# Performance work log

Hardware: AMD Instinct MI355X
Metric: run time of the kernel (lower is better)

The kernel has to match this reference:

```python
import jax, jax.numpy as jnp
import numpy as np

NEG_INF = -1.0e9  # matches torch masked_fill_ value


def setup_inputs() -> dict:
    key = jax.random.key(0)
    kq, kk, kv, km = jax.random.split(key, 4)
    B, H, S, D = 4, 16, 2048, 64
    Q = jax.random.normal(kq, (B, H, S, D), dtype=jnp.float32)
    K = jax.random.normal(kk, (B, H, S, D), dtype=jnp.float32)
    V = jax.random.normal(kv, (B, H, S, D), dtype=jnp.float32)
    attn_mask = jax.random.randint(km, (B, 1, 1, S), 0, 2).astype(jnp.bool_)
    return {"Q": Q, "K": K, "V": V, "attn_mask": attn_mask}


def reference(Q, K, V, attn_mask):
    d_k = Q.shape[-1]
    scale = 1.0 / jnp.sqrt(jnp.asarray(d_k, dtype=Q.dtype))
    # scores: [B, H, Sq, Sk]
    scores = jnp.einsum('bhqd,bhkd->bhqk', Q, K) * scale
    scores = jnp.where(attn_mask, jnp.asarray(NEG_INF, dtype=scores.dtype), scores)
    attn = jax.nn.softmax(scores, axis=-1)
    context = jnp.einsum('bhqk,bhkd->bhqd', attn, V)
    return (context, attn)
```

## Files before the change

### kernel.cpp

```cpp
#include <hip/hip_runtime.h>
#include <stdint.h>

#define B_    4
#define H_    16
#define S_    2048
#define D_    64
#define SCALE_LOG2E 0.1803368801111244f

typedef __bf16 bf16x8 __attribute__((ext_vector_type(8)));
typedef __bf16 bf16x4 __attribute__((ext_vector_type(4)));
typedef float  f32x4  __attribute__((ext_vector_type(4)));

__global__ __launch_bounds__(256)
void prep_k(const float* __restrict__ K, __bf16* __restrict__ img) {
    int t = blockIdx.x * 256 + threadIdx.x;
    int C = t & 255, slice = t >> 8;
    int sb = slice & 1, e = (slice >> 1) & 31, bh = slice >> 6;
    int l15 = C & 15, lhi = (C >> 4) & 3, kd = (C >> 6) & 1, ksub = C >> 7;
    const float* src = K + (((size_t)bh * S_ + e * 64 + sb * 32 + ksub * 16 + l15) * D_
                            + kd * 32 + lhi * 8);
    float4 a = *reinterpret_cast<const float4*>(src);
    float4 b = *reinterpret_cast<const float4*>(src + 4);
    bf16x8 w = { (__bf16)a.x,(__bf16)a.y,(__bf16)a.z,(__bf16)a.w,
                 (__bf16)b.x,(__bf16)b.y,(__bf16)b.z,(__bf16)b.w };
    *reinterpret_cast<bf16x8*>((char*)img + ((size_t)t << 4)) = w;
}

__global__ __launch_bounds__(256)
void prep_v(const float* __restrict__ V, __bf16* __restrict__ img) {
    __shared__ float Ls[64][65];
    const int tid = threadIdx.x;
    const int bh = blockIdx.x >> 5, e = blockIdx.x & 31;
    const float* Vp = V + ((size_t)bh * S_ + e * 64) * D_;
    for (int i = tid; i < 1024; i += 256) {
        int r = i >> 4, c = (i & 15) << 2;
        float4 v = reinterpret_cast<const float4*>(Vp)[i];
        Ls[r][c] = v.x; Ls[r][c+1] = v.y; Ls[r][c+2] = v.z; Ls[r][c+3] = v.w;
    }
    __syncthreads();
    char* base = (char*)img + (size_t)(bh * 32 + e) * 8192;
    #pragma unroll
    for (int m = tid; m < 512; m += 256) {
        int sb = m >> 8, C2 = m & 255;
        int db = C2 >> 6, lhi = (C2 >> 4) & 3, l15 = C2 & 15;
        bf16x8 w;
        #pragma unroll
        for (int j = 0; j < 8; ++j)
            w[j] = (__bf16)Ls[sb * 32 + lhi * 4 + (j & 3) + ((j >> 2) << 4)][db * 16 + l15];
        *reinterpret_cast<bf16x8*>(base + sb * 4096 + C2 * 16) = w;
    }
}

__global__ __launch_bounds__(256, 2)
void sdpa_main(const float* __restrict__ Q, const __bf16* __restrict__ Kimg,
               const __bf16* __restrict__ Vimg, const int* __restrict__ mask,
               float* __restrict__ ctx_out, float* __restrict__ attn_out)
{
    __shared__ __align__(16) float shbuf[64 * 65];

    const int tid  = threadIdx.x;
    const int lane = tid & 63, wid = tid >> 6;
    const int l15  = lane & 15, lhi = lane >> 4;
    const int par  = wid & 1;
    const int sb   = wid >> 1;

    const int orig = blockIdx.x, cpx = gridDim.x >> 3;
    const int bid  = (orig & 7) * cpx + (orig >> 3);
    const int qt = bid & 31, bh = bid >> 5, b = bh >> 4;

    const char* kimgT = (const char*)Kimg + (size_t)bh * 262144;
    const char* vimgT = (const char*)Vimg + (size_t)bh * 262144;

    bf16x8 bQ[4][2];
    #pragma unroll
    for (int rb = 0; rb < 4; ++rb) {
        const float* qrow = Q + ((size_t)bh * S_ + qt * 64 + rb * 16 + l15) * D_ + lhi * 8;
        float4 a = *reinterpret_cast<const float4*>(qrow);
        float4 c = *reinterpret_cast<const float4*>(qrow + 4);
        bf16x8 w0 = { (__bf16)(a.x*SCALE_LOG2E),(__bf16)(a.y*SCALE_LOG2E),
                      (__bf16)(a.z*SCALE_LOG2E),(__bf16)(a.w*SCALE_LOG2E),
                      (__bf16)(c.x*SCALE_LOG2E),(__bf16)(c.y*SCALE_LOG2E),
                      (__bf16)(c.z*SCALE_LOG2E),(__bf16)(c.w*SCALE_LOG2E) };
        bQ[rb][0] = w0;
        a = *reinterpret_cast<const float4*>(qrow + 32);
        c = *reinterpret_cast<const float4*>(qrow + 36);
        bf16x8 w1 = { (__bf16)(a.x*SCALE_LOG2E),(__bf16)(a.y*SCALE_LOG2E),
                      (__bf16)(a.z*SCALE_LOG2E),(__bf16)(a.w*SCALE_LOG2E),
                      (__bf16)(c.x*SCALE_LOG2E),(__bf16)(c.y*SCALE_LOG2E),
                      (__bf16)(c.z*SCALE_LOG2E),(__bf16)(c.w*SCALE_LOG2E) };
        bQ[rb][1] = w1;
    }

    uint32_t mwv[4] = {0, 0, 0, 0};
    {
        const int* mrow = mask + b * S_ + sb * 32 + lhi * 4;
        #pragma unroll
        for (int tt = 0; tt < 16; ++tt) {
            int e = (((tt + qt) & 15) << 1) | par;
            #pragma unroll
            for (int ksub = 0; ksub < 2; ++ksub) {
                int4 mm = *reinterpret_cast<const int4*>(mrow + e * 64 + ksub * 16);
                uint32_t nib = (mm.x ? 1u : 0u) | (mm.y ? 2u : 0u) |
                               (mm.z ? 4u : 0u) | (mm.w ? 8u : 0u);
                mwv[tt >> 2] |= nib << (((tt & 3) * 8) + ksub * 4);
            }
        }
    }

    bf16x8 kf[2][2][2];
    auto loadK = [&](int bufi, int tt) {
        int e = (((tt + qt) & 15) << 1) | par;
        const char* p = kimgT + (size_t)(e * 2 + sb) * 4096 + lane * 16;
        kf[bufi][0][0] = *reinterpret_cast<const bf16x8*>(p);
        kf[bufi][0][1] = *reinterpret_cast<const bf16x8*>(p + 1024);
        kf[bufi][1][0] = *reinterpret_cast<const bf16x8*>(p + 2048);
        kf[bufi][1][1] = *reinterpret_cast<const bf16x8*>(p + 3072);
    };
    bf16x8 vv[2][4];
    auto loadV = [&](int bufi, int tt) {
        int e = (((tt + qt) & 15) << 1) | par;
        const char* p = vimgT + (size_t)(e * 2 + sb) * 4096 + lane * 16;
        vv[bufi][0] = *reinterpret_cast<const bf16x8*>(p);
        vv[bufi][1] = *reinterpret_cast<const bf16x8*>(p + 1024);
        vv[bufi][2] = *reinterpret_cast<const bf16x8*>(p + 2048);
        vv[bufi][3] = *reinterpret_cast<const bf16x8*>(p + 3072);
    };

    float ls[4] = {0.f, 0.f, 0.f, 0.f};
    loadK(0, 0);
    #pragma unroll
    for (int tt = 0; tt < 16; ++tt) {
        if (tt + 1 < 16) loadK((tt + 1) & 1, tt + 1);
        const int cur = tt & 1;
        #pragma unroll
        for (int ksub = 0; ksub < 2; ++ksub) {
            uint32_t nib = (mwv[tt >> 2] >> (((tt & 3) * 8) + ksub * 4)) & 15u;
            #pragma unroll
            for (int rb = 0; rb < 4; ++rb) {
                f32x4 acc = {0.f, 0.f, 0.f, 0.f};
                acc = __builtin_amdgcn_mfma_f32_16x16x32_bf16(kf[cur][ksub][0], bQ[rb][0], acc, 0, 0, 0);
                acc = __builtin_amdgcn_mfma_f32_16x16x32_bf16(kf[cur][ksub][1], bQ[rb][1], acc, 0, 0, 0);
                float p0 = (nib & 1u) ? 0.f : exp2f(acc[0]);
                float p1 = (nib & 2u) ? 0.f : exp2f(acc[1]);
                float p2 = (nib & 4u) ? 0.f : exp2f(acc[2]);
                float p3 = (nib & 8u) ? 0.f : exp2f(acc[3]);
                ls[rb] += (p0 + p1) + (p2 + p3);
            }
        }
    }

    #pragma unroll
    for (int rb = 0; rb < 4; ++rb) {
        ls[rb] += __shfl_xor(ls[rb], 16);
        ls[rb] += __shfl_xor(ls[rb], 32);
    }
    if (lhi == 0) {
        #pragma unroll
        for (int rb = 0; rb < 4; ++rb) shbuf[(wid * 4 + rb) * 16 + l15] = ls[rb];
    }
    __syncthreads();
    float rl[4];
    #pragma unroll
    for (int rb = 0; rb < 4; ++rb) {
        float tot = (shbuf[rb * 16 + l15] + shbuf[(4 + rb) * 16 + l15]) +
                    (shbuf[(8 + rb) * 16 + l15] + shbuf[(12 + rb) * 16 + l15]);
        rl[rb] = 1.0f / tot;
    }

    f32x4 ctx[4][4];
    #pragma unroll
    for (int rb = 0; rb < 4; ++rb)
        #pragma unroll
        for (int db = 0; db < 4; ++db) ctx[rb][db] = (f32x4){0.f, 0.f, 0.f, 0.f};

    const size_t arowq = (size_t)bh * S_ + (size_t)qt * 64;

    loadK(0, 0); loadV(0, 0);
    bf16x4 pk[2][4];
    #pragma unroll
    for (int tt = 0; tt < 16; ++tt) {
        if (tt + 1 < 16) { loadK((tt + 1) & 1, tt + 1); loadV((tt + 1) & 1, tt + 1); }
        const int cur = tt & 1;
        const int e = (((tt + qt) & 15) << 1) | par;
        const int colbase = e * 64 + sb * 32;
        #pragma unroll
        for (int rb = 0; rb < 4; ++rb) {
            float* arow = attn_out + (arowq + rb * 16 + l15) * S_ + colbase + lhi * 4;
            #pragma unroll
            for (int ksub = 0; ksub < 2; ++ksub) {
                uint32_t nib = (mwv[tt >> 2] >> (((tt & 3) * 8) + ksub * 4)) & 15u;
                f32x4 acc = {0.f, 0.f, 0.f, 0.f};
                acc = __builtin_amdgcn_mfma_f32_16x16x32_bf16(kf[cur][ksub][0], bQ[rb][0], acc, 0, 0, 0);
                acc = __builtin_amdgcn_mfma_f32_16x16x32_bf16(kf[cur][ksub][1], bQ[rb][1], acc, 0, 0, 0);
                float p0 = (nib & 1u) ? 0.f : exp2f(acc[0]) * rl[rb];
                float p1 = (nib & 2u) ? 0.f : exp2f(acc[1]) * rl[rb];
                float p2 = (nib & 4u) ? 0.f : exp2f(acc[2]) * rl[rb];
                float p3 = (nib & 8u) ? 0.f : exp2f(acc[3]) * rl[rb];
                float4 st = { p0, p1, p2, p3 };
                *reinterpret_cast<float4*>(arow + ksub * 16) = st;
                bf16x4 pkk = { (__bf16)p0, (__bf16)p1, (__bf16)p2, (__bf16)p3 };
                pk[ksub][rb] = pkk;
            }
        }
        #pragma unroll
        for (int db = 0; db < 4; ++db) {
            #pragma unroll
            for (int rb = 0; rb < 4; ++rb) {
                bf16x8 Av;
                Av[0]=pk[0][rb][0]; Av[1]=pk[0][rb][1]; Av[2]=pk[0][rb][2]; Av[3]=pk[0][rb][3];
                Av[4]=pk[1][rb][0]; Av[5]=pk[1][rb][1]; Av[6]=pk[1][rb][2]; Av[7]=pk[1][rb][3];
                ctx[rb][db] = __builtin_amdgcn_mfma_f32_16x16x32_bf16(Av, vv[cur][db], ctx[rb][db], 0, 0, 0);
            }
        }
    }

    __syncthreads();
    for (int ph = 0; ph < 4; ++ph) {
        if (wid == ph) {
            #pragma unroll
            for (int rb = 0; rb < 4; ++rb)
                #pragma unroll
                for (int db = 0; db < 4; ++db)
                    #pragma unroll
                    for (int r = 0; r < 4; ++r) {
                        float* c = &shbuf[(rb * 16 + lhi * 4 + r) * 65 + db * 16 + l15];
                        if (ph == 0) *c = ctx[rb][db][r];
                        else         *c += ctx[rb][db][r];
                    }
        }
        __syncthreads();
    }
    for (int i = tid; i < 4096; i += 256) {
        int q = i >> 6, d = i & 63;
        ctx_out[(arowq + q) * D_ + d] = shbuf[q * 65 + d];
    }
}

extern "C" void kernel_launch(void* const* d_in, const int* in_sizes, int n_in,
                              void* d_out, int out_size, void* d_ws, size_t ws_size,
                              hipStream_t stream) {
    const float* Q    = (const float*)d_in[0];
    const float* K    = (const float*)d_in[1];
    const float* V    = (const float*)d_in[2];
    const int*   mask = (const int*)d_in[3];

    float* ctx_out  = (float*)d_out;
    float* attn_out = ctx_out + (size_t)B_ * H_ * S_ * D_;

    __bf16* Kimg = (__bf16*)d_ws;
    __bf16* Vimg = Kimg + (size_t)B_ * H_ * S_ * D_;

    prep_k<<<4096, 256, 0, stream>>>(K, Kimg);
    prep_v<<<B_ * H_ * 32, 256, 0, stream>>>(V, Vimg);
    sdpa_main<<<B_ * H_ * 32, 256, 0, stream>>>(Q, Kimg, Vimg, mask, ctx_out, attn_out);
}
```

Baseline: 438.2 us.

## Restructure attention into single-wave blocks over 16 query rows each

Replaces the 256-thread block, in which four waves split the keys of 64 queries and reduce through shared memory, with 64-thread blocks where one wave handles 16 query rows across all keys. This removes the shared-memory row-sum and context reductions and their barriers, and launches four times as many blocks. The attention-probability stores become nontemporal. The trade-off is that each wave now re-reads the full K and V for only 16 queries, so cache traffic per query goes up.

```diff
diff --git a/kernel.cpp b/kernel.cpp
--- a/kernel.cpp
+++ b/kernel.cpp
@@ -51,188 +51,192 @@
     }
 }
 
-__global__ __launch_bounds__(256, 2)
+__global__ __launch_bounds__(64, 3)
 void sdpa_main(const float* __restrict__ Q, const __bf16* __restrict__ Kimg,
                const __bf16* __restrict__ Vimg, const int* __restrict__ mask,
                float* __restrict__ ctx_out, float* __restrict__ attn_out)
 {
-    __shared__ __align__(16) float shbuf[64 * 65];
-
-    const int tid  = threadIdx.x;
-    const int lane = tid & 63, wid = tid >> 6;
-    const int l15  = lane & 15, lhi = lane >> 4;
-    const int par  = wid & 1;
-    const int sb   = wid >> 1;
-
-    const int orig = blockIdx.x, cpx = gridDim.x >> 3;
-    const int bid  = (orig & 7) * cpx + (orig >> 3);
-    const int qt = bid & 31, bh = bid >> 5, b = bh >> 4;
+    const int lane = threadIdx.x;
+    const int l15 = lane & 15, lhi = lane >> 4;
+
+    const int orig = blockIdx.x;
+    const int bid = (orig & 7) * (int)(gridDim.x >> 3) + (orig >> 3);
+    const int q16 = bid & 127, bh = bid >> 7, b = bh >> 4;
 
     const char* kimgT = (const char*)Kimg + (size_t)bh * 262144;
     const char* vimgT = (const char*)Vimg + (size_t)bh * 262144;
 
-    bf16x8 bQ[4][2];
-    #pragma unroll
-    for (int rb = 0; rb < 4; ++rb) {
-        const float* qrow = Q + ((size_t)bh * S_ + qt * 64 + rb * 16 + l15) * D_ + lhi * 8;
+    bf16x8 bQ0, bQ1;
+    {
+        const float* qrow = Q + ((size_t)bh * S_ + q16 * 16 + l15) * D_ + lhi * 8;
         float4 a = *reinterpret_cast<const float4*>(qrow);
         float4 c = *reinterpret_cast<const float4*>(qrow + 4);
-        bf16x8 w0 = { (__bf16)(a.x*SCALE_LOG2E),(__bf16)(a.y*SCALE_LOG2E),
-                      (__bf16)(a.z*SCALE_LOG2E),(__bf16)(a.w*SCALE_LOG2E),
-                      (__bf16)(c.x*SCALE_LOG2E),(__bf16)(c.y*SCALE_LOG2E),
-                      (__bf16)(c.z*SCALE_LOG2E),(__bf16)(c.w*SCALE_LOG2E) };
-        bQ[rb][0] = w0;
+        bQ0 = (bf16x8){ (__bf16)(a.x*SCALE_LOG2E),(__bf16)(a.y*SCALE_LOG2E),
+                        (__bf16)(a.z*SCALE_LOG2E),(__bf16)(a.w*SCALE_LOG2E),
+                        (__bf16)(c.x*SCALE_LOG2E),(__bf16)(c.y*SCALE_LOG2E),
+                        (__bf16)(c.z*SCALE_LOG2E),(__bf16)(c.w*SCALE_LOG2E) };
         a = *reinterpret_cast<const float4*>(qrow + 32);
         c = *reinterpret_cast<const float4*>(qrow + 36);
-        bf16x8 w1 = { (__bf16)(a.x*SCALE_LOG2E),(__bf16)(a.y*SCALE_LOG2E),
-                      (__bf16)(a.z*SCALE_LOG2E),(__bf16)(a.w*SCALE_LOG2E),
-                      (__bf16)(c.x*SCALE_LOG2E),(__bf16)(c.y*SCALE_LOG2E),
-                      (__bf16)(c.z*SCALE_LOG2E),(__bf16)(c.w*SCALE_LOG2E) };
-        bQ[rb][1] = w1;
-    }
-
-    uint32_t mwv[4] = {0, 0, 0, 0};
+        bQ1 = (bf16x8){ (__bf16)(a.x*SCALE_LOG2E),(__bf16)(a.y*SCALE_LOG2E),
+                        (__bf16)(a.z*SCALE_LOG2E),(__bf16)(a.w*SCALE_LOG2E),
+                        (__bf16)(c.x*SCALE_LOG2E),(__bf16)(c.y*SCALE_LOG2E),
+                        (__bf16)(c.z*SCALE_LOG2E),(__bf16)(c.w*SCALE_LOG2E) };
+    }
+
+    uint32_t mA0,mA1,mA2,mA3, mB0,mB1,mB2,mB3, mC0,mC1,mC2,mC3, mD0,mD1,mD2,mD3;
     {
-        const int* mrow = mask + b * S_ + sb * 32 + lhi * 4;
+        const int* mb2 = mask + b * S_ + lhi * 4;
+        auto packw = [&](int tw, uint32_t& a, uint32_t& bb, uint32_t& cc, uint32_t& dd) {
+            a = bb = cc = dd = 0;
+            #pragma unroll
+            for (int u = 0; u < 8; ++u) {
+                int e = (tw * 8 + u + q16) & 31;
+                const int* p = mb2 + e * 64;
+                int4 m0 = *reinterpret_cast<const int4*>(p);
+                int4 m1 = *reinterpret_cast<const int4*>(p + 16);
+                int4 m2 = *reinterpret_cast<const int4*>(p + 32);
+                int4 m3 = *reinterpret_cast<const int4*>(p + 48);
+                uint32_t nA = (m0.x?1u:0u)|(m0.y?2u:0u)|(m0.z?4u:0u)|(m0.w?8u:0u);
+                uint32_t nB = (m1.x?1u:0u)|(m1.y?2u:0u)|(m1.z?4u:0u)|(m1.w?8u:0u);
+                uint32_t nC = (m2.x?1u:0u)|(m2.y?2u:0u)|(m2.z?4u:0u)|(m2.w?8u:0u);
+                uint32_t nD = (m3.x?1u:0u)|(m3.y?2u:0u)|(m3.z?4u:0u)|(m3.w?8u:0u);
+                a |= nA << (u*4); bb |= nB << (u*4); cc |= nC << (u*4); dd |= nD << (u*4);
+            }
+        };
+        packw(0, mA0, mB0, mC0, mD0);
+        packw(1, mA1, mB1, mC1, mD1);
+        packw(2, mA2, mB2, mC2, mD2);
+        packw(3, mA3, mB3, mC3, mD3);
+    }
+
+    bf16x8 kf[2][2][2];
+    auto loadK = [&](int tt) {
+        int e = (tt + q16) & 31;
+        const char* p0 = kimgT + (size_t)(e * 2) * 4096 + lane * 16;
+        kf[0][0][0] = *reinterpret_cast<const bf16x8*>(p0);
+        kf[0][0][1] = *reinterpret_cast<const bf16x8*>(p0 + 1024);
+        kf[0][1][0] = *reinterpret_cast<const bf16x8*>(p0 + 2048);
+        kf[0][1][1] = *reinterpret_cast<const bf16x8*>(p0 + 3072);
+        const char* p1 = p0 + 4096;
+        kf[1][0][0] = *reinterpret_cast<const bf16x8*>(p1);
+        kf[1][0][1] = *reinterpret_cast<const bf16x8*>(p1 + 1024);
+        kf[1][1][0] = *reinterpret_cast<const bf16x8*>(p1 + 2048);
+        kf[1][1][1] = *reinterpret_cast<const bf16x8*>(p1 + 3072);
+    };
+    bf16x8 vv[2][4];
+    auto loadV = [&](int tt) {
+        int e = (tt + q16) & 31;
+        const char* p0 = vimgT + (size_t)(e * 2) * 4096 + lane * 16;
+        vv[0][0] = *reinterpret_cast<const bf16x8*>(p0);
+        vv[0][1] = *reinterpret_cast<const bf16x8*>(p0 + 1024);
+        vv[0][2] = *reinterpret_cast<const bf16x8*>(p0 + 2048);
+        vv[0][3] = *reinterpret_cast<const bf16x8*>(p0 + 3072);
+        const char* p1 = p0 + 4096;
+        vv[1][0] = *reinterpret_cast<const bf16x8*>(p1);
+        vv[1][1] = *reinterpret_cast<const bf16x8*>(p1 + 1024);
+        vv[1][2] = *reinterpret_cast<const bf16x8*>(p1 + 2048);
+        vv[1][3] = *reinterpret_cast<const bf16x8*>(p1 + 3072);
+    };
+
+    float ls = 0.f;
+    loadK(0);
+    auto sumExp = [&](const f32x4& acc, uint32_t nib) -> float {
+        float p0 = (nib & 1u) ? 0.f : exp2f(acc[0]);
+        float p1 = (nib & 2u) ? 0.f : exp2f(acc[1]);
+        float p2 = (nib & 4u) ? 0.f : exp2f(acc[2]);
+        float p3 = (nib & 8u) ? 0.f : exp2f(acc[3]);
+        return (p0 + p1) + (p2 + p3);
+    };
+    auto pass1_8 = [&](int tw, uint32_t mA, uint32_t mB, uint32_t mC, uint32_t mD) {
+        #pragma unroll 2
+        for (int u = 0; u < 8; ++u) {
+            int tt = tw * 8 + u;
+            f32x4 z = {0.f,0.f,0.f,0.f};
+            f32x4 a00 = __builtin_amdgcn_mfma_f32_16x16x32_bf16(kf[0][0][0], bQ0, z, 0,0,0);
+            a00 = __builtin_amdgcn_mfma_f32_16x16x32_bf16(kf[0][0][1], bQ1, a00, 0,0,0);
+            f32x4 a01 = __builtin_amdgcn_mfma_f32_16x16x32_bf16(kf[0][1][0], bQ0, z, 0,0,0);
+            a01 = __builtin_amdgcn_mfma_f32_16x16x32_bf16(kf[0][1][1], bQ1, a01, 0,0,0);
+            f32x4 a10 = __builtin_amdgcn_mfma_f32_16x16x32_bf16(kf[1][0][0], bQ0, z, 0,0,0);
+            a10 = __builtin_amdgcn_mfma_f32_16x16x32_bf16(kf[1][0][1], bQ1, a10, 0,0,0);
+            f32x4 a11 = __builtin_amdgcn_mfma_f32_16x16x32_bf16(kf[1][1][0], bQ0, z, 0,0,0);
+            a11 = __builtin_amdgcn_mfma_f32_16x16x32_bf16(kf[1][1][1], bQ1, a11, 0,0,0);
+            loadK((tt + 1) & 31);
+            int sh = u * 4;
+            ls += sumExp(a00, (mA >> sh) & 15u) + sumExp(a01, (mB >> sh) & 15u)
+                + sumExp(a10, (mC >> sh) & 15u) + sumExp(a11, (mD >> sh) & 15u);
+        }
+    };
+    pass1_8(0, mA0, mB0, mC0, mD0);
+    pass1_8(1, mA1, mB1, mC1, mD1);
+    pass1_8(2, mA2, mB2, mC2, mD2);
+    pass1_8(3, mA3, mB3, mC3, mD3);
+
+    ls += __shfl_xor(ls, 16);
+    ls += __shfl_xor(ls, 32);
+    const float rl = 1.0f / ls;
+
+    f32x4 ctx[4];
+    #pragma unroll
+    for (int db = 0; db < 4; ++db) ctx[db] = (f32x4){0.f,0.f,0.f,0.f};
+
+    const size_t arow0 = (size_t)bh * S_ + (size_t)q16 * 16;
+    float* arowp = attn_out + (arow0 + l15) * S_ + lhi * 4;
+
+    loadK(0); loadV(0);
+    auto pass2_8 = [&](int tw, uint32_t mA, uint32_t mB, uint32_t mC, uint32_t mD) {
+        #pragma unroll 2
+        for (int u = 0; u < 8; ++u) {
+            int tt = tw * 8 + u;
+            int e = (tt + q16) & 31;
+            f32x4 z = {0.f,0.f,0.f,0.f};
+            f32x4 a00 = __builtin_amdgcn_mfma_f32_16x16x32_bf16(kf[0][0][0], bQ0, z, 0,0,0);
+            a00 = __builtin_amdgcn_mfma_f32_16x16x32_bf16(kf[0][0][1], bQ1, a00, 0,0,0);
+            f32x4 a01 = __builtin_amdgcn_mfma_f32_16x16x32_bf16(kf[0][1][0], bQ0, z, 0,0,0);
+            a01 = __builtin_amdgcn_mfma_f32_16x16x32_bf16(kf[0][1][1], bQ1, a01, 0,0,0);
+            f32x4 a10 = __builtin_amdgcn_mfma_f32_16x16x32_bf16(kf[1][0][0], bQ0, z, 0,0,0);
+            a10 = __builtin_amdgcn_mfma_f32_16x16x32_bf16(kf[1][0][1], bQ1, a10, 0,0,0);
+            f32x4 a11 = __builtin_amdgcn_mfma_f32_16x16x32_bf16(kf[1][1][0], bQ0, z, 0,0,0);
+            a11 = __builtin_amdgcn_mfma_f32_16x16x32_bf16(kf[1][1][1], bQ1, a11, 0,0,0);
+            loadK((tt + 1) & 31);
+            int sh = u * 4;
+            uint32_t nA = (mA >> sh) & 15u, nB = (mB >> sh) & 15u;
+            uint32_t nC = (mC >> sh) & 15u, nD = (mD >> sh) & 15u;
+            f32x4 sA = { (nA&1u)?0.f:exp2f(a00[0])*rl, (nA&2u)?0.f:exp2f(a00[1])*rl,
+                         (nA&4u)?0.f:exp2f(a00[2])*rl, (nA&8u)?0.f:exp2f(a00[3])*rl };
+            f32x4 sB = { (nB&1u)?0.f:exp2f(a01[0])*rl, (nB&2u)?0.f:exp2f(a01[1])*rl,
+                         (nB&4u)?0.f:exp2f(a01[2])*rl, (nB&8u)?0.f:exp2f(a01[3])*rl };
+            f32x4 sC = { (nC&1u)?0.f:exp2f(a10[0])*rl, (nC&2u)?0.f:exp2f(a10[1])*rl,
+                         (nC&4u)?0.f:exp2f(a10[2])*rl, (nC&8u)?0.f:exp2f(a10[3])*rl };
+            f32x4 sD = { (nD&1u)?0.f:exp2f(a11[0])*rl, (nD&2u)?0.f:exp2f(a11[1])*rl,
+                         (nD&4u)?0.f:exp2f(a11[2])*rl, (nD&8u)?0.f:exp2f(a11[3])*rl };
+            float* ap = arowp + e * 64;
+            __builtin_nontemporal_store(sA, reinterpret_cast<f32x4*>(ap));
+            __builtin_nontemporal_store(sB, reinterpret_cast<f32x4*>(ap + 16));
+            __builtin_nontemporal_store(sC, reinterpret_cast<f32x4*>(ap + 32));
+            __builtin_nontemporal_store(sD, reinterpret_cast<f32x4*>(ap + 48));
+            bf16x8 Av0 = { (__bf16)sA[0],(__bf16)sA[1],(__bf16)sA[2],(__bf16)sA[3],
+                           (__bf16)sB[0],(__bf16)sB[1],(__bf16)sB[2],(__bf16)sB[3] };
+            bf16x8 Av1 = { (__bf16)sC[0],(__bf16)sC[1],(__bf16)sC[2],(__bf16)sC[3],
+                           (__bf16)sD[0],(__bf16)sD[1],(__bf16)sD[2],(__bf16)sD[3] };
+            #pragma unroll
+            for (int db = 0; db < 4; ++db) {
+                ctx[db] = __builtin_amdgcn_mfma_f32_16x16x32_bf16(Av0, vv[0][db], ctx[db], 0,0,0);
+                ctx[db] = __builtin_amdgcn_mfma_f32_16x16x32_bf16(Av1, vv[1][db], ctx[db], 0,0,0);
+            }
+            loadV((tt + 1) & 31);
+        }
+    };
+    pass2_8(0, mA0, mB0, mC0, mD0);
+    pass2_8(1, mA1, mB1, mC1, mD1);
+    pass2_8(2, mA2, mB2, mC2, mD2);
+    pass2_8(3, mA3, mB3, mC3, mD3);
+
+    #pragma unroll
+    for (int db = 0; db < 4; ++db) {
         #pragma unroll
-        for (int tt = 0; tt < 16; ++tt) {
-            int e = (((tt + qt) & 15) << 1) | par;
-            #pragma unroll
-            for (int ksub = 0; ksub < 2; ++ksub) {
-                int4 mm = *reinterpret_cast<const int4*>(mrow + e * 64 + ksub * 16);
-                uint32_t nib = (mm.x ? 1u : 0u) | (mm.y ? 2u : 0u) |
-                               (mm.z ? 4u : 0u) | (mm.w ? 8u : 0u);
-                mwv[tt >> 2] |= nib << (((tt & 3) * 8) + ksub * 4);
-            }
+        for (int r = 0; r < 4; ++r) {
+            ctx_out[(arow0 + lhi * 4 + r) * D_ + db * 16 + l15] = ctx[db][r];
         }
-    }
-
-    bf16x8 kf[2][2][2];
-    auto loadK = [&](int bufi, int tt) {
-        int e = (((tt + qt) & 15) << 1) | par;
-        const char* p = kimgT + (size_t)(e * 2 + sb) * 4096 + lane * 16;
-        kf[bufi][0][0] = *reinterpret_cast<const bf16x8*>(p);
-        kf[bufi][0][1] = *reinterpret_cast<const bf16x8*>(p + 1024);
-        kf[bufi][1][0] = *reinterpret_cast<const bf16x8*>(p + 2048);
-        kf[bufi][1][1] = *reinterpret_cast<const bf16x8*>(p + 3072);
-    };
-    bf16x8 vv[2][4];
-    auto loadV = [&](int bufi, int tt) {
-        int e = (((tt + qt) & 15) << 1) | par;
-        const char* p = vimgT + (size_t)(e * 2 + sb) * 4096 + lane * 16;
-        vv[bufi][0] = *reinterpret_cast<const bf16x8*>(p);
-        vv[bufi][1] = *reinterpret_cast<const bf16x8*>(p + 1024);
-        vv[bufi][2] = *reinterpret_cast<const bf16x8*>(p + 2048);
-        vv[bufi][3] = *reinterpret_cast<const bf16x8*>(p + 3072);
-    };
-
-    float ls[4] = {0.f, 0.f, 0.f, 0.f};
-    loadK(0, 0);
-    #pragma unroll
-    for (int tt = 0; tt < 16; ++tt) {
-        if (tt + 1 < 16) loadK((tt + 1) & 1, tt + 1);
-        const int cur = tt & 1;
-        #pragma unroll
-        for (int ksub = 0; ksub < 2; ++ksub) {
-            uint32_t nib = (mwv[tt >> 2] >> (((tt & 3) * 8) + ksub * 4)) & 15u;
-            #pragma unroll
-            for (int rb = 0; rb < 4; ++rb) {
-                f32x4 acc = {0.f, 0.f, 0.f, 0.f};
-                acc = __builtin_amdgcn_mfma_f32_16x16x32_bf16(kf[cur][ksub][0], bQ[rb][0], acc, 0, 0, 0);
-                acc = __builtin_amdgcn_mfma_f32_16x16x32_bf16(kf[cur][ksub][1], bQ[rb][1], acc, 0, 0, 0);
-                float p0 = (nib & 1u) ? 0.f : exp2f(acc[0]);
-                float p1 = (nib & 2u) ? 0.f : exp2f(acc[1]);
-                float p2 = (nib & 4u) ? 0.f : exp2f(acc[2]);
-                float p3 = (nib & 8u) ? 0.f : exp2f(acc[3]);
-                ls[rb] += (p0 + p1) + (p2 + p3);
-            }
-        }
-    }
-
-    #pragma unroll
-    for (int rb = 0; rb < 4; ++rb) {
-        ls[rb] += __shfl_xor(ls[rb], 16);
-        ls[rb] += __shfl_xor(ls[rb], 32);
-    }
-    if (lhi == 0) {
-        #pragma unroll
-        for (int rb = 0; rb < 4; ++rb) shbuf[(wid * 4 + rb) * 16 + l15] = ls[rb];
-    }
-    __syncthreads();
-    float rl[4];
-    #pragma unroll
-    for (int rb = 0; rb < 4; ++rb) {
-        float tot = (shbuf[rb * 16 + l15] + shbuf[(4 + rb) * 16 + l15]) +
-                    (shbuf[(8 + rb) * 16 + l15] + shbuf[(12 + rb) * 16 + l15]);
-        rl[rb] = 1.0f / tot;
-    }
-
-    f32x4 ctx[4][4];
-    #pragma unroll
-    for (int rb = 0; rb < 4; ++rb)
-        #pragma unroll
-        for (int db = 0; db < 4; ++db) ctx[rb][db] = (f32x4){0.f, 0.f, 0.f, 0.f};
-
-    const size_t arowq = (size_t)bh * S_ + (size_t)qt * 64;
-
-    loadK(0, 0); loadV(0, 0);
-    bf16x4 pk[2][4];
-    #pragma unroll
-    for (int tt = 0; tt < 16; ++tt) {
-        if (tt + 1 < 16) { loadK((tt + 1) & 1, tt + 1); loadV((tt + 1) & 1, tt + 1); }
-        const int cur = tt & 1;
-        const int e = (((tt + qt) & 15) << 1) | par;
-        const int colbase = e * 64 + sb * 32;
-        #pragma unroll
-        for (int rb = 0; rb < 4; ++rb) {
-            float* arow = attn_out + (arowq + rb * 16 + l15) * S_ + colbase + lhi * 4;
-            #pragma unroll
-            for (int ksub = 0; ksub < 2; ++ksub) {
-                uint32_t nib = (mwv[tt >> 2] >> (((tt & 3) * 8) + ksub * 4)) & 15u;
-                f32x4 acc = {0.f, 0.f, 0.f, 0.f};
-                acc = __builtin_amdgcn_mfma_f32_16x16x32_bf16(kf[cur][ksub][0], bQ[rb][0], acc, 0, 0, 0);
-                acc = __builtin_amdgcn_mfma_f32_16x16x32_bf16(kf[cur][ksub][1], bQ[rb][1], acc, 0, 0, 0);
-                float p0 = (nib & 1u) ? 0.f : exp2f(acc[0]) * rl[rb];
-                float p1 = (nib & 2u) ? 0.f : exp2f(acc[1]) * rl[rb];
-                float p2 = (nib & 4u) ? 0.f : exp2f(acc[2]) * rl[rb];
-                float p3 = (nib & 8u) ? 0.f : exp2f(acc[3]) * rl[rb];
-                float4 st = { p0, p1, p2, p3 };
-                *reinterpret_cast<float4*>(arow + ksub * 16) = st;
-                bf16x4 pkk = { (__bf16)p0, (__bf16)p1, (__bf16)p2, (__bf16)p3 };
-                pk[ksub][rb] = pkk;
-            }
-        }
-        #pragma unroll
-        for (int db = 0; db < 4; ++db) {
-            #pragma unroll
-            for (int rb = 0; rb < 4; ++rb) {
-                bf16x8 Av;
-                Av[0]=pk[0][rb][0]; Av[1]=pk[0][rb][1]; Av[2]=pk[0][rb][2]; Av[3]=pk[0][rb][3];
-                Av[4]=pk[1][rb][0]; Av[5]=pk[1][rb][1]; Av[6]=pk[1][rb][2]; Av[7]=pk[1][rb][3];
-                ctx[rb][db] = __builtin_amdgcn_mfma_f32_16x16x32_bf16(Av, vv[cur][db], ctx[rb][db], 0, 0, 0);
-            }
-        }
-    }
-
-    __syncthreads();
-    for (int ph = 0; ph < 4; ++ph) {
-        if (wid == ph) {
-            #pragma unroll
-            for (int rb = 0; rb < 4; ++rb)
-                #pragma unroll
-                for (int db = 0; db < 4; ++db)
-                    #pragma unroll
-                    for (int r = 0; r < 4; ++r) {
-                        float* c = &shbuf[(rb * 16 + lhi * 4 + r) * 65 + db * 16 + l15];
-                        if (ph == 0) *c = ctx[rb][db][r];
-                        else         *c += ctx[rb][db][r];
-                    }
-        }
-        __syncthreads();
-    }
-    for (int i = tid; i < 4096; i += 256) {
-        int q = i >> 6, d = i & 63;
-        ctx_out[(arowq + q) * D_ + d] = shbuf[q * 65 + d];
     }
 }
 
@@ -252,5 +256,5 @@
 
     prep_k<<<4096, 256, 0, stream>>>(K, Kimg);
     prep_v<<<B_ * H_ * 32, 256, 0, stream>>>(V, Vimg);
-    sdpa_main<<<B_ * H_ * 32, 256, 0, stream>>>(Q, Kimg, Vimg, mask, ctx_out, attn_out);
-}
+    sdpa_main<<<B_ * H_ * 128, 64, 0, stream>>>(Q, Kimg, Vimg, mask, ctx_out, attn_out);
+}
```

Result: slower. 841.4 us (+92.0%).

## Stage attention probabilities through swizzled LDS for coalesced full-row attn stores

Applied to the files above, without the earlier changes.

Instead of each lane writing scattered float4 pieces of the attention matrix directly to global memory, probabilities are written into a 32KB XOR-swizzled shared-memory tile (one 16KB half per key parity). After a barrier, each wave reads back contiguous 256-byte row segments and stores them coalesced. This targets write efficiency on the dominant attn output traffic, at the cost of more shared memory (which may lower occupancy) and two extra block barriers per key tile.

```diff
diff --git a/kernel.cpp b/kernel.cpp
--- a/kernel.cpp
+++ b/kernel.cpp
@@ -56,7 +56,7 @@
                const __bf16* __restrict__ Vimg, const int* __restrict__ mask,
                float* __restrict__ ctx_out, float* __restrict__ attn_out)
 {
-    __shared__ __align__(16) float shbuf[64 * 65];
+    __shared__ __align__(16) char smem[32768];
 
     const int tid  = threadIdx.x;
     const int lane = tid & 63, wid = tid >> 6;
@@ -77,18 +77,16 @@
         const float* qrow = Q + ((size_t)bh * S_ + qt * 64 + rb * 16 + l15) * D_ + lhi * 8;
         float4 a = *reinterpret_cast<const float4*>(qrow);
         float4 c = *reinterpret_cast<const float4*>(qrow + 4);
-        bf16x8 w0 = { (__bf16)(a.x*SCALE_LOG2E),(__bf16)(a.y*SCALE_LOG2E),
-                      (__bf16)(a.z*SCALE_LOG2E),(__bf16)(a.w*SCALE_LOG2E),
-                      (__bf16)(c.x*SCALE_LOG2E),(__bf16)(c.y*SCALE_LOG2E),
-                      (__bf16)(c.z*SCALE_LOG2E),(__bf16)(c.w*SCALE_LOG2E) };
-        bQ[rb][0] = w0;
+        bQ[rb][0] = (bf16x8){ (__bf16)(a.x*SCALE_LOG2E),(__bf16)(a.y*SCALE_LOG2E),
+                              (__bf16)(a.z*SCALE_LOG2E),(__bf16)(a.w*SCALE_LOG2E),
+                              (__bf16)(c.x*SCALE_LOG2E),(__bf16)(c.y*SCALE_LOG2E),
+                              (__bf16)(c.z*SCALE_LOG2E),(__bf16)(c.w*SCALE_LOG2E) };
         a = *reinterpret_cast<const float4*>(qrow + 32);
         c = *reinterpret_cast<const float4*>(qrow + 36);
-        bf16x8 w1 = { (__bf16)(a.x*SCALE_LOG2E),(__bf16)(a.y*SCALE_LOG2E),
-                      (__bf16)(a.z*SCALE_LOG2E),(__bf16)(a.w*SCALE_LOG2E),
-                      (__bf16)(c.x*SCALE_LOG2E),(__bf16)(c.y*SCALE_LOG2E),
-                      (__bf16)(c.z*SCALE_LOG2E),(__bf16)(c.w*SCALE_LOG2E) };
-        bQ[rb][1] = w1;
+        bQ[rb][1] = (bf16x8){ (__bf16)(a.x*SCALE_LOG2E),(__bf16)(a.y*SCALE_LOG2E),
+                              (__bf16)(a.z*SCALE_LOG2E),(__bf16)(a.w*SCALE_LOG2E),
+                              (__bf16)(c.x*SCALE_LOG2E),(__bf16)(c.y*SCALE_LOG2E),
+                              (__bf16)(c.z*SCALE_LOG2E),(__bf16)(c.w*SCALE_LOG2E) };
     }
 
     uint32_t mwv[4] = {0, 0, 0, 0};
@@ -154,26 +152,29 @@
         ls[rb] += __shfl_xor(ls[rb], 16);
         ls[rb] += __shfl_xor(ls[rb], 32);
     }
+    float* lsb = reinterpret_cast<float*>(smem);
     if (lhi == 0) {
         #pragma unroll
-        for (int rb = 0; rb < 4; ++rb) shbuf[(wid * 4 + rb) * 16 + l15] = ls[rb];
+        for (int rb = 0; rb < 4; ++rb) lsb[(wid * 4 + rb) * 16 + l15] = ls[rb];
     }
     __syncthreads();
     float rl[4];
     #pragma unroll
     for (int rb = 0; rb < 4; ++rb) {
-        float tot = (shbuf[rb * 16 + l15] + shbuf[(4 + rb) * 16 + l15]) +
-                    (shbuf[(8 + rb) * 16 + l15] + shbuf[(12 + rb) * 16 + l15]);
+        float tot = (lsb[rb * 16 + l15] + lsb[(4 + rb) * 16 + l15]) +
+                    (lsb[(8 + rb) * 16 + l15] + lsb[(12 + rb) * 16 + l15]);
         rl[rb] = 1.0f / tot;
     }
+    __syncthreads();
 
     f32x4 ctx[4][4];
     #pragma unroll
     for (int rb = 0; rb < 4; ++rb)
         #pragma unroll
-        for (int db = 0; db < 4; ++db) ctx[rb][db] = (f32x4){0.f, 0.f, 0.f, 0.f};
+        for (int db = 0; db < 4; ++db) ctx[rb][db] = (f32x4){0.f,0.f,0.f,0.f};
 
     const size_t arowq = (size_t)bh * S_ + (size_t)qt * 64;
+    char* psPar = smem + (par << 14);
 
     loadK(0, 0); loadV(0, 0);
     bf16x4 pk[2][4];
@@ -182,10 +183,9 @@
         if (tt + 1 < 16) { loadK((tt + 1) & 1, tt + 1); loadV((tt + 1) & 1, tt + 1); }
         const int cur = tt & 1;
         const int e = (((tt + qt) & 15) << 1) | par;
-        const int colbase = e * 64 + sb * 32;
         #pragma unroll
         for (int rb = 0; rb < 4; ++rb) {
-            float* arow = attn_out + (arowq + rb * 16 + l15) * S_ + colbase + lhi * 4;
+            const int q = rb * 16 + l15;
             #pragma unroll
             for (int ksub = 0; ksub < 2; ++ksub) {
                 uint32_t nib = (mwv[tt >> 2] >> (((tt & 3) * 8) + ksub * 4)) & 15u;
@@ -196,10 +196,10 @@
                 float p1 = (nib & 2u) ? 0.f : exp2f(acc[1]) * rl[rb];
                 float p2 = (nib & 4u) ? 0.f : exp2f(acc[2]) * rl[rb];
                 float p3 = (nib & 8u) ? 0.f : exp2f(acc[3]) * rl[rb];
-                float4 st = { p0, p1, p2, p3 };
-                *reinterpret_cast<float4*>(arow + ksub * 16) = st;
-                bf16x4 pkk = { (__bf16)p0, (__bf16)p1, (__bf16)p2, (__bf16)p3 };
-                pk[ksub][rb] = pkk;
+                f32x4 st = { p0, p1, p2, p3 };
+                int chunk = ((sb << 3) + (ksub << 2) + lhi) ^ (q & 15);
+                *reinterpret_cast<f32x4*>(psPar + q * 256 + (chunk << 4)) = st;
+                pk[ksub][rb] = (bf16x4){ (__bf16)p0, (__bf16)p1, (__bf16)p2, (__bf16)p3 };
             }
         }
         #pragma unroll
@@ -212,9 +212,18 @@
                 ctx[rb][db] = __builtin_amdgcn_mfma_f32_16x16x32_bf16(Av, vv[cur][db], ctx[rb][db], 0, 0, 0);
             }
         }
-    }
-
-    __syncthreads();
+        __syncthreads();
+        #pragma unroll
+        for (int it = 0; it < 8; ++it) {
+            int row = sb * 32 + it * 4 + lhi;
+            f32x4 v = *reinterpret_cast<f32x4*>(psPar + row * 256 + ((l15 ^ (row & 15)) << 4));
+            *reinterpret_cast<f32x4*>(attn_out + (arowq + row) * S_ + e * 64 + l15 * 4) = v;
+        }
+        __syncthreads();
+    }
+
+    __syncthreads();
+    float* Cred = reinterpret_cast<float*>(smem);
     for (int ph = 0; ph < 4; ++ph) {
         if (wid == ph) {
             #pragma unroll
@@ -223,7 +232,7 @@
                 for (int db = 0; db < 4; ++db)
                     #pragma unroll
                     for (int r = 0; r < 4; ++r) {
-                        float* c = &shbuf[(rb * 16 + lhi * 4 + r) * 65 + db * 16 + l15];
+                        float* c = &Cred[(rb * 16 + lhi * 4 + r) * 65 + db * 16 + l15];
                         if (ph == 0) *c = ctx[rb][db][r];
                         else         *c += ctx[rb][db][r];
                     }
@@ -232,7 +241,7 @@
     }
     for (int i = tid; i < 4096; i += 256) {
         int q = i >> 6, d = i & 63;
-        ctx_out[(arowq + q) * D_ + d] = shbuf[q * 65 + d];
+        ctx_out[(arowq + q) * D_ + d] = Cred[q * 65 + d];
     }
 }
 
```

Measured after the change: 653.9 us. +49.2%, slower.
